# Kernel optimization log

Measured on AMD Instinct MI355X. Metric: run time of the kernel, lower is better.

Reference implementation:

```python
import jax, jax.numpy as jnp
import numpy as np

B, C, H, W = 8, 256, 128, 128
KC, VC, HEADS = 256, 256, 2
HK, HV = KC // HEADS, VC // HEADS
EPS = 1e-5


def setup_inputs() -> dict:
    key = jax.random.key(0)
    ks = jax.random.split(key, 10)
    s = 0.02  # init scale for weights
    return {
        "x": jax.random.normal(ks[0], (B, C, H, W), jnp.float32),
        "bn_gamma": jnp.ones((C,), jnp.float32),
        "bn_beta": jnp.zeros((C,), jnp.float32),
        "wk": jax.random.normal(ks[1], (KC, C), jnp.float32) * s,
        "bk": jnp.zeros((KC,), jnp.float32),
        "wq": jax.random.normal(ks[2], (KC, C), jnp.float32) * s,
        "bq": jnp.zeros((KC,), jnp.float32),
        "wv": jax.random.normal(ks[3], (VC, C), jnp.float32) * s,
        "bv": jnp.zeros((VC,), jnp.float32),
        "w_fc1": jax.random.normal(ks[4], (HEADS, HEADS), jnp.float32) * 0.5,
        "b_fc1": jnp.zeros((HEADS,), jnp.float32),
        "w_fc2": jax.random.normal(ks[5], (HEADS, HEADS), jnp.float32) * 0.5,
        "b_fc2": jnp.zeros((HEADS,), jnp.float32),
        "w_se": jax.random.normal(ks[6], (HEADS,), jnp.float32) * 0.5,  # Conv2d(heads,1,1) weight
        "b_se": jnp.zeros((), jnp.float32),
        "w_rep": jax.random.normal(ks[7], (C, C), jnp.float32) * s,
        "b_rep": jnp.zeros((C,), jnp.float32),
    }


def reference(x, bn_gamma, bn_beta, wk, bk, wq, bq, wv, bv,
              w_fc1, b_fc1, w_fc2, b_fc2, w_se, b_se, w_rep, b_rep):
    n, c, h, w = x.shape
    s = h * w
    # BatchNorm2d (training-mode math: batch statistics over N,H,W)
    mean = x.mean(axis=(0, 2, 3))
    var = x.var(axis=(0, 2, 3))
    xn = (x - mean[None, :, None, None]) * jax.lax.rsqrt(var + EPS)[None, :, None, None]
    xn = xn * bn_gamma[None, :, None, None] + bn_beta[None, :, None, None]
    xr = xn.reshape(n, c, s)  # [B, C, HW]
    # 1x1 convs == per-pixel channel matmuls
    k = jnp.einsum('oc,bcs->bos', wk, xr) + bk[None, :, None]
    q = jnp.einsum('oc,bcs->bos', wq, xr) + bq[None, :, None]
    v = jnp.einsum('oc,bcs->bos', wv, xr) + bv[None, :, None]
    # split heads: [B, HEADS, hk, S]
    k = jax.nn.softmax(k.reshape(n, HEADS, HK, s), axis=-1)   # softmax over spatial
    q = jax.nn.softmax(q.reshape(n, HEADS, HK, s), axis=2)    # softmax over channel
    v = v.reshape(n, HEADS, HV, s)
    # linear-attention context: key @ value^T -> [B, HEADS, hk, hv]
    context = jnp.einsum('bnks,bnvs->bnkv', k, v)
    # SE block over head channel (in_channels = HEADS, reduction = 1)
    pooled = context.mean(axis=(2, 3))                              # [B, HEADS]
    gate = jax.nn.sigmoid(jax.nn.relu(pooled @ w_fc1.T + b_fc1) @ w_fc2.T + b_fc2)
    gated = context * gate[:, :, None, None]
    ctx = jnp.einsum('n,bnkv->bkv', w_se, gated) + b_se             # Conv2d(HEADS,1,1): [B, hk, hv]
    # second pass: ctx^T @ query per head, concat over heads -> [B, C, S]
    out = jnp.einsum('bkv,bnks->bnvs', ctx, q).reshape(n, c, s)
    out = jnp.einsum('oc,bcs->bos', w_rep, out) + b_rep[None, :, None]
    return out.reshape(n, c, h, w)
```

## Files before the change

### kernel.cpp

```cpp
#include <hip/hip_runtime.h>
#include <hip/hip_bf16.h>

#define BATCH 8
#define CH 256
#define SPAT 16384
#define TP 64
#define PITCH 272

typedef __attribute__((ext_vector_type(4))) float f32x4;
typedef __attribute__((ext_vector_type(8))) __bf16 bf16x8;
typedef __attribute__((ext_vector_type(4))) __bf16 bf16x4;

#define WS_ROWSUM  512
#define WS_POOLED  2560
#define WS_BKF     2576
#define WS_BQF     2832
#define WS_BVF     3088
#define WS_SUM     3344
#define WS_SSUM    3600
#define WS_CTX     4096
#define WS_MBF     266240
#define WS_WKBF    528384
#define WS_WQBF    561152
#define WS_WVBF    593920

__device__ __forceinline__ int lswz(int h) { return h ^ (((h >> 7) & 7) << 3); }

__device__ __forceinline__ void blockReduce2(float& a, float& b, volatile float* sm) {
    int lane = threadIdx.x & 63, w = threadIdx.x >> 6;
#pragma unroll
    for (int o = 32; o; o >>= 1) { a += __shfl_down(a, o); b += __shfl_down(b, o); }
    if (lane == 0) { sm[w] = a; sm[4 + w] = b; }
    __syncthreads();
    if (threadIdx.x == 0) {
        a = sm[0] + sm[1] + sm[2] + sm[3];
        b = sm[4] + sm[5] + sm[6] + sm[7];
    }
}

__global__ __launch_bounds__(256) void ea_bnstats(const float* __restrict__ x,
                                                  float* sums, float* ssums) {
    __shared__ float sm[8];
    int bi = blockIdx.x, c = bi >> 3, b = bi & 7;
    const float4* p = (const float4*)(x + (size_t)(b * CH + c) * SPAT);
    float sum = 0.f, ss = 0.f;
    for (int i = threadIdx.x; i < SPAT / 4; i += 256) {
        float4 v = p[i];
        sum += v.x + v.y + v.z + v.w;
        ss  += v.x * v.x + v.y * v.y + v.z * v.z + v.w * v.w;
    }
    blockReduce2(sum, ss, sm);
    if (threadIdx.x == 0) { atomicAdd(sums + c, sum); atomicAdd(ssums + c, ss); }
}

__global__ __launch_bounds__(256) void ea_fold(const float* __restrict__ wk, const float* __restrict__ wq,
        const float* __restrict__ wv, const float* __restrict__ bk, const float* __restrict__ bq,
        const float* __restrict__ bv, const float* __restrict__ gamma, const float* __restrict__ beta,
        const float* __restrict__ sums, const float* __restrict__ ssums,
        __bf16* wkb, __bf16* wqb, __bf16* wvb, float* bkf, float* bqf, float* bvf) {
    __shared__ float sm[12];
    int o = blockIdx.x, c = threadIdx.x;
    const float inv = 1.f / (float)(BATCH * SPAT);
    float mean = sums[c] * inv;
    float var  = ssums[c] * inv - mean * mean;
    float sc   = gamma[c] * rsqrtf(var + 1e-5f);
    float sh   = beta[c] - mean * sc;
    float k = wk[o * 256 + c], q = wq[o * 256 + c], v = wv[o * 256 + c];
    wkb[o * 256 + c] = (__bf16)(k * sc);
    wqb[o * 256 + c] = (__bf16)(q * sc);
    wvb[o * 256 + c] = (__bf16)(v * sc);
    float ak = k * sh, aq = q * sh, av = v * sh;
    int lane = c & 63, w = c >> 6;
#pragma unroll
    for (int off = 32; off; off >>= 1) {
        ak += __shfl_down(ak, off);
        aq += __shfl_down(aq, off);
        av += __shfl_down(av, off);
    }
    if (lane == 0) { sm[w] = ak; sm[4 + w] = aq; sm[8 + w] = av; }
    __syncthreads();
    if (c == 0) {
        bkf[o] = bk[o] + sm[0] + sm[1] + sm[2] + sm[3];
        bqf[o] = bq[o] + sm[4] + sm[5] + sm[6] + sm[7];
        bvf[o] = bv[o] + sm[8] + sm[9] + sm[10] + sm[11];
    }
}

__device__ __forceinline__ void stage_x(const float* xb, __bf16* Xl, int t) {
    int l15 = t & 15, c0 = t >> 4;
    const float* xp = xb + l15 * 4;
    int hbase = (l15 * 4) * PITCH;
#pragma unroll
    for (int i = 0; i < 16; i++) {
        int c = c0 * 16 + i;
        float4 v = *(const float4*)(xp + (size_t)c * SPAT);
        Xl[lswz(hbase + c)]             = (__bf16)v.x;
        Xl[lswz(hbase + PITCH + c)]     = (__bf16)v.y;
        Xl[lswz(hbase + 2 * PITCH + c)] = (__bf16)v.z;
        Xl[lswz(hbase + 3 * PITCH + c)] = (__bf16)v.w;
    }
}

__device__ __forceinline__ void mm256(const __bf16* __restrict__ A, const __bf16* Xl,
                                      int WB, int quad, int l15, f32x4 (&acc)[4][4]) {
#pragma unroll 2
    for (int ks = 0; ks < 8; ks++) {
        int k0 = ks * 32;
        bf16x8 a[4];
#pragma unroll
        for (int mt = 0; mt < 4; mt++)
            a[mt] = *(const bf16x8*)(A + (WB + mt * 16 + l15) * 256 + k0 + quad * 8);
        bf16x8 bb[4];
#pragma unroll
        for (int nt = 0; nt < 4; nt++)
            bb[nt] = *(const bf16x8*)(Xl + lswz((4 * l15 + nt) * PITCH + k0 + quad * 8));
#pragma unroll
        for (int mt = 0; mt < 4; mt++)
#pragma unroll
            for (int nt = 0; nt < 4; nt++)
                acc[mt][nt] = __builtin_amdgcn_mfma_f32_16x16x32_bf16(a[mt], bb[nt], acc[mt][nt], 0, 0, 0);
    }
}

__global__ __launch_bounds__(256) void ea_projkv(const float* __restrict__ x,
        const __bf16* __restrict__ wkb, const __bf16* __restrict__ wvb,
        const float* __restrict__ bkf, const float* __restrict__ bvf,
        __bf16* __restrict__ pbuf, __bf16* __restrict__ vbuf, float* __restrict__ rowsum) {
    __shared__ __bf16 X[TP * PITCH];
    int bi = blockIdx.x, b = bi >> 8, s0 = (bi & 255) * TP, t = threadIdx.x;
    stage_x(x + (size_t)b * CH * SPAT + s0, X, t);
    __syncthreads();

    int lane = t & 63, wave = t >> 6, quad = lane >> 4, l15 = lane & 15, WB = wave * 64;
    const f32x4 z = {0.f, 0.f, 0.f, 0.f};

    {
        f32x4 acc[4][4];
#pragma unroll
        for (int mt = 0; mt < 4; mt++)
#pragma unroll
            for (int nt = 0; nt < 4; nt++) acc[mt][nt] = z;
        mm256(wkb, X, WB, quad, l15, acc);
#pragma unroll
        for (int mt = 0; mt < 4; mt++) {
            int row0 = WB + mt * 16 + quad * 4;
#pragma unroll
            for (int r = 0; r < 4; r++) {
                int row = row0 + r;
                float bs = bkf[row];
                float e0 = __expf(acc[mt][0][r] + bs);
                float e1 = __expf(acc[mt][1][r] + bs);
                float e2 = __expf(acc[mt][2][r] + bs);
                float e3 = __expf(acc[mt][3][r] + bs);
                bf16x4 pk = {(__bf16)e0, (__bf16)e1, (__bf16)e2, (__bf16)e3};
                *(bf16x4*)(pbuf + (size_t)(b * CH + row) * SPAT + s0 + 4 * l15) = pk;
                float rs = e0 + e1 + e2 + e3;
#pragma unroll
                for (int o = 1; o < 16; o <<= 1) rs += __shfl_xor(rs, o);
                if (l15 == 0) atomicAdd(rowsum + b * CH + row, rs);
            }
        }
    }
    {
        f32x4 acc[4][4];
#pragma unroll
        for (int mt = 0; mt < 4; mt++)
#pragma unroll
            for (int nt = 0; nt < 4; nt++) acc[mt][nt] = z;
        mm256(wvb, X, WB, quad, l15, acc);
#pragma unroll
        for (int mt = 0; mt < 4; mt++) {
            int row0 = WB + mt * 16 + quad * 4;
#pragma unroll
            for (int r = 0; r < 4; r++) {
                int row = row0 + r;
                float bs = bvf[row];
                bf16x4 vk = {(__bf16)(acc[mt][0][r] + bs), (__bf16)(acc[mt][1][r] + bs),
                             (__bf16)(acc[mt][2][r] + bs), (__bf16)(acc[mt][3][r] + bs)};
                *(bf16x4*)(vbuf + (size_t)(b * CH + row) * SPAT + s0 + 4 * l15) = vk;
            }
        }
    }
}

__global__ __launch_bounds__(256) void ea_context(const __bf16* pbuf, const __bf16* vbuf, float* ctx) {
    int bi = blockIdx.x, b = bi >> 5, h = (bi >> 4) & 1, chunk = bi & 15;
    int sb = chunk * 1024;
    int t = threadIdx.x, lane = t & 63, wave = t >> 6, quad = lane >> 4, l15 = lane & 15;
    int WB = wave * 32;
    const __bf16* pb = pbuf + (size_t)(b * CH + h * 128) * SPAT;
    const __bf16* vb = vbuf + (size_t)(b * CH + h * 128) * SPAT;
    const f32x4 z = {0.f, 0.f, 0.f, 0.f};
    f32x4 acc[2][8];
#pragma unroll
    for (int mt = 0; mt < 2; mt++)
#pragma unroll
        for (int nt = 0; nt < 8; nt++) acc[mt][nt] = z;

#pragma unroll 2
    for (int ks = 0; ks < 32; ks++) {
        int k0 = sb + ks * 32;
        bf16x8 a[2];
#pragma unroll
        for (int mt = 0; mt < 2; mt++)
            a[mt] = *(const bf16x8*)(pb + (size_t)(WB + mt * 16 + l15) * SPAT + k0 + quad * 8);
        bf16x8 bb[8];
#pragma unroll
        for (int nt = 0; nt < 8; nt++)
            bb[nt] = *(const bf16x8*)(vb + (size_t)(nt * 16 + l15) * SPAT + k0 + quad * 8);
#pragma unroll
        for (int mt = 0; mt < 2; mt++)
#pragma unroll
            for (int nt = 0; nt < 8; nt++)
                acc[mt][nt] = __builtin_amdgcn_mfma_f32_16x16x32_bf16(a[mt], bb[nt], acc[mt][nt], 0, 0, 0);
    }
    float* cbase = ctx + (size_t)(b * 2 + h) * 16384;
#pragma unroll
    for (int mt = 0; mt < 2; mt++)
#pragma unroll
        for (int nt = 0; nt < 8; nt++)
#pragma unroll
            for (int r = 0; r < 4; r++) {
                int kk = WB + mt * 16 + quad * 4 + r, vv = nt * 16 + l15;
                atomicAdd(cbase + kk * 128 + vv, acc[mt][nt][r]);
            }
}

__global__ void ea_normpool(float* ctx, const float* rowsum, float* pooled) {
    __shared__ float sm[8];
    int bi = blockIdx.x, b = bi >> 1, h = bi & 1;
    float* base = ctx + (size_t)bi * 16384;
    const float* rs = rowsum + b * CH + h * 128;
    float sum = 0.f, dummy = 0.f;
    for (int i = threadIdx.x; i < 16384; i += 256) {
        float v = base[i] / rs[i >> 7];
        base[i] = v;
        sum += v;
    }
    blockReduce2(sum, dummy, sm);
    if (threadIdx.x == 0) pooled[bi] = sum * (1.f / 16384.f);
}

__global__ __launch_bounds__(256) void ea_M(const float* ctx, const float* pooled,
                                            const float* wfc1, const float* bfc1,
                                            const float* wfc2, const float* bfc2,
                                            const float* wse, const float* bse,
                                            const float* wrep, __bf16* Mbf) {
    __shared__ float L[128 * 128];
    int bi = blockIdx.x, b = bi >> 3, h = (bi >> 2) & 1, strip = bi & 3;
    float p0 = pooled[b * 2], p1 = pooled[b * 2 + 1];
    float z10 = fmaxf(0.f, wfc1[0] * p0 + wfc1[1] * p1 + bfc1[0]);
    float z11 = fmaxf(0.f, wfc1[2] * p0 + wfc1[3] * p1 + bfc1[1]);
    float z20 = wfc2[0] * z10 + wfc2[1] * z11 + bfc2[0];
    float z21 = wfc2[2] * z10 + wfc2[3] * z11 + bfc2[1];
    float g0 = 1.f / (1.f + __expf(-z20)), g1 = 1.f / (1.f + __expf(-z21));
    float a0 = wse[0] * g0, a1 = wse[1] * g1, bs = bse[0];
    const float* c0 = ctx + (size_t)b * 2 * 16384;
    const float* c1 = c0 + 16384;
    for (int i = threadIdx.x; i < 16384; i += 256) L[i] = a0 * c0[i] + a1 * c1[i] + bs;
    __syncthreads();
    int o = strip * 64 + (threadIdx.x & 63), kb = (threadIdx.x >> 6) * 32;
    const float4* wr = (const float4*)(wrep + (size_t)o * 256 + h * 128);
    for (int kk = kb; kk < kb + 32; kk++) {
        const float4* Lr = (const float4*)(L + kk * 128);
        float acc = 0.f;
#pragma unroll 8
        for (int j = 0; j < 32; j++) {
            float4 w4 = wr[j];
            float4 l4 = Lr[j];
            acc += w4.x * l4.x + w4.y * l4.y + w4.z * l4.z + w4.w * l4.w;
        }
        Mbf[(size_t)(b * 256 + o) * 256 + h * 128 + kk] = (__bf16)acc;
    }
}

__global__ __launch_bounds__(256) void ea_final(const float* __restrict__ x,
        const __bf16* __restrict__ wqb, const float* __restrict__ bqf,
        const __bf16* __restrict__ Mbf, const float* __restrict__ brep, float* __restrict__ out) {
    __shared__ __bf16 X[TP * PITCH];
    __shared__ __bf16 Q[TP * PITCH];
    __shared__ float psum[256];
    __shared__ float rcp[TP * 2];
    int bi = blockIdx.x, b = bi >> 8, s0 = (bi & 255) * TP, t = threadIdx.x;
    stage_x(x + (size_t)b * CH * SPAT + s0, X, t);
    __syncthreads();

    int lane = t & 63, wave = t >> 6, quad = lane >> 4, l15 = lane & 15, WB = wave * 64;
    const f32x4 z = {0.f, 0.f, 0.f, 0.f};

    {
        f32x4 acc[4][4];
#pragma unroll
        for (int mt = 0; mt < 4; mt++)
#pragma unroll
            for (int nt = 0; nt < 4; nt++) acc[mt][nt] = z;
        mm256(wqb, X, WB, quad, l15, acc);
#pragma unroll
        for (int mt = 0; mt < 4; mt++) {
            int row0 = WB + mt * 16 + quad * 4;
#pragma unroll
            for (int nt = 0; nt < 4; nt++) {
                bf16x4 qk;
#pragma unroll
                for (int r = 0; r < 4; r++)
                    qk[r] = (__bf16)__expf(acc[mt][nt][r] + bqf[row0 + r]);
                *(bf16x4*)(Q + lswz((4 * l15 + nt) * PITCH + row0)) = qk;
            }
        }
    }
    __syncthreads();
    {
        int px = t & 63, hh = (t >> 6) & 1, part = t >> 7;
        int cb = hh * 128 + part * 64;
        float s = 0.f;
#pragma unroll
        for (int j = 0; j < 8; j++) {
            bf16x8 qv = *(const bf16x8*)(Q + lswz(px * PITCH + cb + j * 8));
#pragma unroll
            for (int e = 0; e < 8; e++) s += (float)qv[e];
        }
        psum[t] = s;
    }
    __syncthreads();
    if (t < 128) {
        float tot = psum[t] + psum[t + 128];
        rcp[(t & 63) * 2 + (t >> 6)] = 1.f / tot;
    }
    __syncthreads();
#pragma unroll 2
    for (int e = t; e < TP * 32; e += 256) {
        int px = e >> 5, cc = (e & 31) * 8;
        float sc = rcp[px * 2 + (cc >> 7)];
        int h = lswz(px * PITCH + cc);
        bf16x8 qv = *(const bf16x8*)(Q + h);
        bf16x8 qo;
#pragma unroll
        for (int j2 = 0; j2 < 8; j2++) qo[j2] = (__bf16)((float)qv[j2] * sc);
        *(bf16x8*)(Q + h) = qo;
    }
    __syncthreads();
    {
        f32x4 acc[4][4];
#pragma unroll
        for (int mt = 0; mt < 4; mt++)
#pragma unroll
            for (int nt = 0; nt < 4; nt++) acc[mt][nt] = z;
        mm256(Mbf + (size_t)b * 65536, Q, WB, quad, l15, acc);
#pragma unroll
        for (int mt = 0; mt < 4; mt++) {
            int row0 = WB + mt * 16 + quad * 4;
#pragma unroll
            for (int r = 0; r < 4; r++) {
                int row = row0 + r;
                float bs = brep[row];
                f32x4 o4 = {acc[mt][0][r] + bs, acc[mt][1][r] + bs,
                            acc[mt][2][r] + bs, acc[mt][3][r] + bs};
                *(f32x4*)(out + (size_t)(b * CH + row) * SPAT + s0 + 4 * l15) = o4;
            }
        }
    }
}

extern "C" void kernel_launch(void* const* d_in, const int* in_sizes, int n_in,
                              void* d_out, int out_size, void* d_ws, size_t ws_size,
                              hipStream_t stream) {
    (void)in_sizes; (void)n_in; (void)out_size; (void)ws_size;
    const float* x     = (const float*)d_in[0];
    const float* gamma = (const float*)d_in[1];
    const float* beta  = (const float*)d_in[2];
    const float* wk    = (const float*)d_in[3];
    const float* bk    = (const float*)d_in[4];
    const float* wq    = (const float*)d_in[5];
    const float* bq    = (const float*)d_in[6];
    const float* wv    = (const float*)d_in[7];
    const float* bv    = (const float*)d_in[8];
    const float* wfc1  = (const float*)d_in[9];
    const float* bfc1  = (const float*)d_in[10];
    const float* wfc2  = (const float*)d_in[11];
    const float* bfc2  = (const float*)d_in[12];
    const float* wse   = (const float*)d_in[13];
    const float* bse   = (const float*)d_in[14];
    const float* wrep  = (const float*)d_in[15];
    const float* brep  = (const float*)d_in[16];

    float* ws = (float*)d_ws;
    __bf16* wkb = (__bf16*)(ws + WS_WKBF);
    __bf16* wqb = (__bf16*)(ws + WS_WQBF);
    __bf16* wvb = (__bf16*)(ws + WS_WVBF);
    __bf16* Mbf = (__bf16*)(ws + WS_MBF);

    __bf16* pbuf = (__bf16*)d_out;
    __bf16* vbuf = pbuf + (size_t)BATCH * CH * SPAT;
    float* out = (float*)d_out;

    hipMemsetAsync((void*)(ws + WS_ROWSUM), 0,
                   (size_t)(WS_MBF - WS_ROWSUM) * sizeof(float), stream);
    ea_bnstats<<<2048, 256, 0, stream>>>(x, ws + WS_SUM, ws + WS_SSUM);
    ea_fold<<<256, 256, 0, stream>>>(wk, wq, wv, bk, bq, bv, gamma, beta,
                                     ws + WS_SUM, ws + WS_SSUM,
                                     wkb, wqb, wvb, ws + WS_BKF, ws + WS_BQF, ws + WS_BVF);
    ea_projkv<<<2048, 256, 0, stream>>>(x, wkb, wvb, ws + WS_BKF, ws + WS_BVF,
                                        pbuf, vbuf, ws + WS_ROWSUM);
    ea_context<<<256, 256, 0, stream>>>(pbuf, vbuf, ws + WS_CTX);
    ea_normpool<<<16, 256, 0, stream>>>(ws + WS_CTX, ws + WS_ROWSUM, ws + WS_POOLED);
    ea_M<<<64, 256, 0, stream>>>(ws + WS_CTX, ws + WS_POOLED, wfc1, bfc1, wfc2, bfc2,
                                 wse, bse, wrep, Mbf);
    ea_final<<<2048, 256, 0, stream>>>(x, wqb, ws + WS_BQF, Mbf, brep, out);
}
```

Baseline: 681.9 us.

## Fuse K/V projection with context accumulation through LDS tiles

Replaces the separate projection and context kernels with one kernel that computes exp(K) and V tiles into shared memory and immediately accumulates P·V^T with MFMA, so the intermediate buffers are never written to or read from global memory. The x tiles are prefetched into registers and double-buffered in LDS across the spatial loop. Row sums are accumulated in registers and reduced once per block. The grid shrinks to 256 blocks of 512 threads, which lowers parallelism and adds more atomics per context element per block.

Result: faster. 604.9 us (-11.3%).

```diff
diff --git a/kernel.cpp b/kernel.cpp
--- a/kernel.cpp
+++ b/kernel.cpp
@@ -86,143 +86,163 @@
     }
 }
 
-__device__ __forceinline__ void stage_x(const float* xb, __bf16* Xl, int t) {
-    int l15 = t & 15, c0 = t >> 4;
-    const float* xp = xb + l15 * 4;
-    int hbase = (l15 * 4) * PITCH;
-#pragma unroll
-    for (int i = 0; i < 16; i++) {
-        int c = c0 * 16 + i;
-        float4 v = *(const float4*)(xp + (size_t)c * SPAT);
-        Xl[lswz(hbase + c)]             = (__bf16)v.x;
-        Xl[lswz(hbase + PITCH + c)]     = (__bf16)v.y;
-        Xl[lswz(hbase + 2 * PITCH + c)] = (__bf16)v.z;
-        Xl[lswz(hbase + 3 * PITCH + c)] = (__bf16)v.w;
-    }
-}
-
-__device__ __forceinline__ void mm256(const __bf16* __restrict__ A, const __bf16* Xl,
-                                      int WB, int quad, int l15, f32x4 (&acc)[4][4]) {
-#pragma unroll 2
-    for (int ks = 0; ks < 8; ks++) {
-        int k0 = ks * 32;
-        bf16x8 a[4];
-#pragma unroll
-        for (int mt = 0; mt < 4; mt++)
-            a[mt] = *(const bf16x8*)(A + (WB + mt * 16 + l15) * 256 + k0 + quad * 8);
-        bf16x8 bb[4];
-#pragma unroll
-        for (int nt = 0; nt < 4; nt++)
-            bb[nt] = *(const bf16x8*)(Xl + lswz((4 * l15 + nt) * PITCH + k0 + quad * 8));
-#pragma unroll
-        for (int mt = 0; mt < 4; mt++)
-#pragma unroll
-            for (int nt = 0; nt < 4; nt++)
-                acc[mt][nt] = __builtin_amdgcn_mfma_f32_16x16x32_bf16(a[mt], bb[nt], acc[mt][nt], 0, 0, 0);
-    }
-}
-
-__global__ __launch_bounds__(256) void ea_projkv(const float* __restrict__ x,
+__global__ __launch_bounds__(512, 2) void ea_kvctx(const float* __restrict__ x,
         const __bf16* __restrict__ wkb, const __bf16* __restrict__ wvb,
         const float* __restrict__ bkf, const float* __restrict__ bvf,
-        __bf16* __restrict__ pbuf, __bf16* __restrict__ vbuf, float* __restrict__ rowsum) {
-    __shared__ __bf16 X[TP * PITCH];
-    int bi = blockIdx.x, b = bi >> 8, s0 = (bi & 255) * TP, t = threadIdx.x;
-    stage_x(x + (size_t)b * CH * SPAT + s0, X, t);
-    __syncthreads();
-
-    int lane = t & 63, wave = t >> 6, quad = lane >> 4, l15 = lane & 15, WB = wave * 64;
+        float* __restrict__ ctx, float* __restrict__ rowsum) {
+    __shared__ __bf16 Xl[2 * 64 * 256];
+    __shared__ __bf16 Pl[256 * 64];
+    __shared__ __bf16 Vl[256 * 64];
+    const int bi = blockIdx.x, b = bi >> 5, chunk = bi & 31;
+    const int t = threadIdx.x;
+    const int lane = t & 63, wave = t >> 6, quad = lane >> 4, l15 = lane & 15;
+    const int rbase = wave * 32;
+    const int sl = t & 15, cg = t >> 4;
+    const int xswz = (sl & 7) << 3;
+    const float* xp0 = x + (size_t)(b * CH + cg * 8) * SPAT + chunk * 512 + 4 * sl;
+
+    float bkr[2][4], bvr[2][4];
+#pragma unroll
+    for (int mt = 0; mt < 2; mt++)
+#pragma unroll
+        for (int r = 0; r < 4; r++) {
+            int row = rbase + mt * 16 + quad * 4 + r;
+            bkr[mt][r] = bkf[row];
+            bvr[mt][r] = bvf[row];
+        }
+
     const f32x4 z = {0.f, 0.f, 0.f, 0.f};
-
-    {
-        f32x4 acc[4][4];
-#pragma unroll
-        for (int mt = 0; mt < 4; mt++)
-#pragma unroll
-            for (int nt = 0; nt < 4; nt++) acc[mt][nt] = z;
-        mm256(wkb, X, WB, quad, l15, acc);
-#pragma unroll
-        for (int mt = 0; mt < 4; mt++) {
-            int row0 = WB + mt * 16 + quad * 4;
+    f32x4 cacc[4][4];
+#pragma unroll
+    for (int mt = 0; mt < 4; mt++)
+#pragma unroll
+        for (int nt = 0; nt < 4; nt++) cacc[mt][nt] = z;
+    float rs_acc[2][4] = {{0.f, 0.f, 0.f, 0.f}, {0.f, 0.f, 0.f, 0.f}};
+
+    const int head = wave >> 2, rh = (wave >> 1) & 1, chh = wave & 1;
+    const int prow0 = head * 128 + rh * 64, vrow0 = head * 128 + chh * 64;
+
+    f32x4 xr[8];
+#pragma unroll
+    for (int i = 0; i < 8; i++) xr[i] = *(const f32x4*)(xp0 + (size_t)i * SPAT);
+#pragma unroll
+    for (int i = 0; i < 8; i++) {
+        int ca = (cg * 8 + i) ^ xswz;
+#pragma unroll
+        for (int j = 0; j < 4; j++)
+            Xl[(4 * sl + j) * 256 + ca] = (__bf16)xr[i][j];
+    }
+    __syncthreads();
+
+    int buf = 0;
+    for (int tt = 0; tt < 8; tt++) {
+        if (tt < 7) {
+            const float* xp = xp0 + (tt + 1) * 64;
+#pragma unroll
+            for (int i = 0; i < 8; i++) xr[i] = *(const f32x4*)(xp + (size_t)i * SPAT);
+        }
+        const __bf16* Xb = Xl + buf * (64 * 256);
+        f32x4 ak[2][4], av[2][4];
+#pragma unroll
+        for (int mt = 0; mt < 2; mt++)
+#pragma unroll
+            for (int nt = 0; nt < 4; nt++) { ak[mt][nt] = z; av[mt][nt] = z; }
+#pragma unroll 1
+        for (int ks = 0; ks < 8; ks++) {
+            int k0 = ks * 32 + quad * 8;
+            bf16x8 bb[4];
+#pragma unroll
+            for (int nt = 0; nt < 4; nt++)
+                bb[nt] = *(const bf16x8*)(Xb + (4 * l15 + nt) * 256 + (k0 ^ ((l15 & 7) << 3)));
+            bf16x8 aK[2], aV[2];
+#pragma unroll
+            for (int mt = 0; mt < 2; mt++) {
+                size_t off = (size_t)(rbase + mt * 16 + l15) * 256 + k0;
+                aK[mt] = *(const bf16x8*)(wkb + off);
+                aV[mt] = *(const bf16x8*)(wvb + off);
+            }
+#pragma unroll
+            for (int mt = 0; mt < 2; mt++)
+#pragma unroll
+                for (int nt = 0; nt < 4; nt++) {
+                    ak[mt][nt] = __builtin_amdgcn_mfma_f32_16x16x32_bf16(aK[mt], bb[nt], ak[mt][nt], 0, 0, 0);
+                    av[mt][nt] = __builtin_amdgcn_mfma_f32_16x16x32_bf16(aV[mt], bb[nt], av[mt][nt], 0, 0, 0);
+                }
+        }
+#pragma unroll
+        for (int mt = 0; mt < 2; mt++)
 #pragma unroll
             for (int r = 0; r < 4; r++) {
-                int row = row0 + r;
-                float bs = bkf[row];
-                float e0 = __expf(acc[mt][0][r] + bs);
-                float e1 = __expf(acc[mt][1][r] + bs);
-                float e2 = __expf(acc[mt][2][r] + bs);
-                float e3 = __expf(acc[mt][3][r] + bs);
+                int row = rbase + mt * 16 + quad * 4 + r;
+                float bK = bkr[mt][r], bV = bvr[mt][r];
+                float e0 = __expf(ak[mt][0][r] + bK);
+                float e1 = __expf(ak[mt][1][r] + bK);
+                float e2 = __expf(ak[mt][2][r] + bK);
+                float e3 = __expf(ak[mt][3][r] + bK);
+                rs_acc[mt][r] += e0 + e1 + e2 + e3;
+                int pa = row * 64 + ((4 * l15) ^ ((row & 7) << 3));
                 bf16x4 pk = {(__bf16)e0, (__bf16)e1, (__bf16)e2, (__bf16)e3};
-                *(bf16x4*)(pbuf + (size_t)(b * CH + row) * SPAT + s0 + 4 * l15) = pk;
-                float rs = e0 + e1 + e2 + e3;
-#pragma unroll
-                for (int o = 1; o < 16; o <<= 1) rs += __shfl_xor(rs, o);
-                if (l15 == 0) atomicAdd(rowsum + b * CH + row, rs);
-            }
-        }
-    }
-    {
-        f32x4 acc[4][4];
-#pragma unroll
-        for (int mt = 0; mt < 4; mt++)
-#pragma unroll
-            for (int nt = 0; nt < 4; nt++) acc[mt][nt] = z;
-        mm256(wvb, X, WB, quad, l15, acc);
-#pragma unroll
-        for (int mt = 0; mt < 4; mt++) {
-            int row0 = WB + mt * 16 + quad * 4;
+                *(bf16x4*)(Pl + pa) = pk;
+                bf16x4 vk = {(__bf16)(av[mt][0][r] + bV), (__bf16)(av[mt][1][r] + bV),
+                             (__bf16)(av[mt][2][r] + bV), (__bf16)(av[mt][3][r] + bV)};
+                *(bf16x4*)(Vl + pa) = vk;
+            }
+        __syncthreads();
+        if (tt < 7) {
+            __bf16* Xn = Xl + (buf ^ 1) * (64 * 256);
+#pragma unroll
+            for (int i = 0; i < 8; i++) {
+                int ca = (cg * 8 + i) ^ xswz;
+#pragma unroll
+                for (int j = 0; j < 4; j++)
+                    Xn[(4 * sl + j) * 256 + ca] = (__bf16)xr[i][j];
+            }
+        }
+#pragma unroll
+        for (int ks = 0; ks < 2; ks++) {
+            int k0 = ks * 32 + quad * 8;
+            bf16x8 pfr[4], vfr[4];
+#pragma unroll
+            for (int mt = 0; mt < 4; mt++) {
+                int row = prow0 + mt * 16 + l15;
+                pfr[mt] = *(const bf16x8*)(Pl + row * 64 + (k0 ^ ((row & 7) << 3)));
+            }
+#pragma unroll
+            for (int nt = 0; nt < 4; nt++) {
+                int row = vrow0 + nt * 16 + l15;
+                vfr[nt] = *(const bf16x8*)(Vl + row * 64 + (k0 ^ ((row & 7) << 3)));
+            }
+#pragma unroll
+            for (int mt = 0; mt < 4; mt++)
+#pragma unroll
+                for (int nt = 0; nt < 4; nt++)
+                    cacc[mt][nt] = __builtin_amdgcn_mfma_f32_16x16x32_bf16(pfr[mt], vfr[nt], cacc[mt][nt], 0, 0, 0);
+        }
+        __syncthreads();
+        buf ^= 1;
+    }
+#pragma unroll
+    for (int mt = 0; mt < 2; mt++)
+#pragma unroll
+        for (int r = 0; r < 4; r++) {
+            float v = rs_acc[mt][r];
+            v += __shfl_xor(v, 1);
+            v += __shfl_xor(v, 2);
+            v += __shfl_xor(v, 4);
+            v += __shfl_xor(v, 8);
+            if (l15 == 0)
+                atomicAdd(rowsum + b * CH + rbase + mt * 16 + quad * 4 + r, v);
+        }
+    float* cb = ctx + ((size_t)b * 2 + head) * 16384;
+#pragma unroll
+    for (int mt = 0; mt < 4; mt++)
+#pragma unroll
+        for (int nt = 0; nt < 4; nt++)
 #pragma unroll
             for (int r = 0; r < 4; r++) {
-                int row = row0 + r;
-                float bs = bvf[row];
-                bf16x4 vk = {(__bf16)(acc[mt][0][r] + bs), (__bf16)(acc[mt][1][r] + bs),
-                             (__bf16)(acc[mt][2][r] + bs), (__bf16)(acc[mt][3][r] + bs)};
-                *(bf16x4*)(vbuf + (size_t)(b * CH + row) * SPAT + s0 + 4 * l15) = vk;
-            }
-        }
-    }
-}
-
-__global__ __launch_bounds__(256) void ea_context(const __bf16* pbuf, const __bf16* vbuf, float* ctx) {
-    int bi = blockIdx.x, b = bi >> 5, h = (bi >> 4) & 1, chunk = bi & 15;
-    int sb = chunk * 1024;
-    int t = threadIdx.x, lane = t & 63, wave = t >> 6, quad = lane >> 4, l15 = lane & 15;
-    int WB = wave * 32;
-    const __bf16* pb = pbuf + (size_t)(b * CH + h * 128) * SPAT;
-    const __bf16* vb = vbuf + (size_t)(b * CH + h * 128) * SPAT;
-    const f32x4 z = {0.f, 0.f, 0.f, 0.f};
-    f32x4 acc[2][8];
-#pragma unroll
-    for (int mt = 0; mt < 2; mt++)
-#pragma unroll
-        for (int nt = 0; nt < 8; nt++) acc[mt][nt] = z;
-
-#pragma unroll 2
-    for (int ks = 0; ks < 32; ks++) {
-        int k0 = sb + ks * 32;
-        bf16x8 a[2];
-#pragma unroll
-        for (int mt = 0; mt < 2; mt++)
-            a[mt] = *(const bf16x8*)(pb + (size_t)(WB + mt * 16 + l15) * SPAT + k0 + quad * 8);
-        bf16x8 bb[8];
-#pragma unroll
-        for (int nt = 0; nt < 8; nt++)
-            bb[nt] = *(const bf16x8*)(vb + (size_t)(nt * 16 + l15) * SPAT + k0 + quad * 8);
-#pragma unroll
-        for (int mt = 0; mt < 2; mt++)
-#pragma unroll
-            for (int nt = 0; nt < 8; nt++)
-                acc[mt][nt] = __builtin_amdgcn_mfma_f32_16x16x32_bf16(a[mt], bb[nt], acc[mt][nt], 0, 0, 0);
-    }
-    float* cbase = ctx + (size_t)(b * 2 + h) * 16384;
-#pragma unroll
-    for (int mt = 0; mt < 2; mt++)
-#pragma unroll
-        for (int nt = 0; nt < 8; nt++)
-#pragma unroll
-            for (int r = 0; r < 4; r++) {
-                int kk = WB + mt * 16 + quad * 4 + r, vv = nt * 16 + l15;
-                atomicAdd(cbase + kk * 128 + vv, acc[mt][nt][r]);
+                int kk = rh * 64 + mt * 16 + quad * 4 + r;
+                int vv = chh * 64 + nt * 16 + l15;
+                atomicAdd(cb + kk * 128 + vv, cacc[mt][nt][r]);
             }
 }
 
@@ -271,6 +291,42 @@
             acc += w4.x * l4.x + w4.y * l4.y + w4.z * l4.z + w4.w * l4.w;
         }
         Mbf[(size_t)(b * 256 + o) * 256 + h * 128 + kk] = (__bf16)acc;
+    }
+}
+
+__device__ __forceinline__ void stage_x(const float* xb, __bf16* Xl, int t) {
+    int l15 = t & 15, c0 = t >> 4;
+    const float* xp = xb + l15 * 4;
+    int hbase = (l15 * 4) * PITCH;
+#pragma unroll
+    for (int i = 0; i < 16; i++) {
+        int c = c0 * 16 + i;
+        float4 v = *(const float4*)(xp + (size_t)c * SPAT);
+        Xl[lswz(hbase + c)]             = (__bf16)v.x;
+        Xl[lswz(hbase + PITCH + c)]     = (__bf16)v.y;
+        Xl[lswz(hbase + 2 * PITCH + c)] = (__bf16)v.z;
+        Xl[lswz(hbase + 3 * PITCH + c)] = (__bf16)v.w;
+    }
+}
+
+__device__ __forceinline__ void mm256(const __bf16* __restrict__ A, const __bf16* Xl,
+                                      int WB, int quad, int l15, f32x4 (&acc)[4][4]) {
+#pragma unroll 2
+    for (int ks = 0; ks < 8; ks++) {
+        int k0 = ks * 32;
+        bf16x8 a[4];
+#pragma unroll
+        for (int mt = 0; mt < 4; mt++)
+            a[mt] = *(const bf16x8*)(A + (WB + mt * 16 + l15) * 256 + k0 + quad * 8);
+        bf16x8 bb[4];
+#pragma unroll
+        for (int nt = 0; nt < 4; nt++)
+            bb[nt] = *(const bf16x8*)(Xl + lswz((4 * l15 + nt) * PITCH + k0 + quad * 8));
+#pragma unroll
+        for (int mt = 0; mt < 4; mt++)
+#pragma unroll
+            for (int nt = 0; nt < 4; nt++)
+                acc[mt][nt] = __builtin_amdgcn_mfma_f32_16x16x32_bf16(a[mt], bb[nt], acc[mt][nt], 0, 0, 0);
     }
 }
 
@@ -388,9 +444,6 @@
     __bf16* wqb = (__bf16*)(ws + WS_WQBF);
     __bf16* wvb = (__bf16*)(ws + WS_WVBF);
     __bf16* Mbf = (__bf16*)(ws + WS_MBF);
-
-    __bf16* pbuf = (__bf16*)d_out;
-    __bf16* vbuf = pbuf + (size_t)BATCH * CH * SPAT;
     float* out = (float*)d_out;
 
     hipMemsetAsync((void*)(ws + WS_ROWSUM), 0,
@@ -399,9 +452,8 @@
     ea_fold<<<256, 256, 0, stream>>>(wk, wq, wv, bk, bq, bv, gamma, beta,
                                      ws + WS_SUM, ws + WS_SSUM,
                                      wkb, wqb, wvb, ws + WS_BKF, ws + WS_BQF, ws + WS_BVF);
-    ea_projkv<<<2048, 256, 0, stream>>>(x, wkb, wvb, ws + WS_BKF, ws + WS_BVF,
-                                        pbuf, vbuf, ws + WS_ROWSUM);
-    ea_context<<<256, 256, 0, stream>>>(pbuf, vbuf, ws + WS_CTX);
+    ea_kvctx<<<256, 512, 0, stream>>>(x, wkb, wvb, ws + WS_BKF, ws + WS_BVF,
+                                      ws + WS_CTX, ws + WS_ROWSUM);
     ea_normpool<<<16, 256, 0, stream>>>(ws + WS_CTX, ws + WS_ROWSUM, ws + WS_POOLED);
     ea_M<<<64, 256, 0, stream>>>(ws + WS_CTX, ws + WS_POOLED, wfc1, bfc1, wfc2, bfc2,
                                  wse, bse, wrep, Mbf);
```
